# Kernel tuning notes

Measured on AMD Instinct MI355X. Metric: run time of the kernel, lower is better.

## Reference

```python
import jax, jax.numpy as jnp
import numpy as np

V = 8192
E = 262144
IN_DIM = 128
OUT_DIM = 128
NEG_SLOPE = 0.2


def setup_inputs() -> dict:
    key = jax.random.key(0)
    k1, k2, k3, k4 = jax.random.split(key, 4)
    h = jax.random.normal(k1, (V, IN_DIM), dtype=jnp.float32)
    edge_index = jax.random.randint(k2, (2, E), 0, V, dtype=jnp.int64)
    # nn.Linear weights: W (out_dim, in_dim), att (1, 2*out_dim), both bias-free
    W = jax.random.normal(k3, (OUT_DIM, IN_DIM), dtype=jnp.float32) / np.sqrt(IN_DIM)
    att_w = jax.random.normal(k4, (1, 2 * OUT_DIM), dtype=jnp.float32) / np.sqrt(2 * OUT_DIM)
    return {"h": h, "edge_index": edge_index, "W": W, "att_w": att_w}


def reference(h, edge_index, W, att_w):
    # h: (V, in_dim) -> (V, out_dim)
    hw = h @ W.T
    src, dst = edge_index[0], edge_index[1]
    # edge features: concat of endpoint embeddings -> (E, 2*out_dim)
    e = jnp.concatenate([hw[src], hw[dst]], axis=-1)
    # attention logits per edge, LeakyReLU(0.2)
    a = jax.nn.leaky_relu(jnp.squeeze(e @ att_w.T, -1), negative_slope=NEG_SLOPE)
    v = hw.shape[0]
    # faithful to original: dense V x V matrix, zeros on non-edges,
    # softmax over ALL columns (non-edges included as score 0)
    alpha = jnp.zeros((v, v), dtype=hw.dtype).at[src, dst].set(a)
    alpha = jax.nn.softmax(alpha, axis=-1)
    # dropout is identity in eval mode (deterministic reference)
    return alpha @ hw
```

## Files before the change

### kernel.cpp

```cpp
#include <hip/hip_runtime.h>
#include <hip/hip_bf16.h>
#include <math.h>


#define V 8192
#define E 262144
#define D 128
#define NEG_SLOPE 0.2f
#define CAP 96

#define FMA4(acc, hv, wv) { acc.x += (hv)*(wv).x; acc.y += (hv)*(wv).y; \
                            acc.z += (hv)*(wv).z; acc.w += (hv)*(wv).w; }

__global__ __launch_bounds__(256) void k_hw(const float* __restrict__ h,
                                            const float* __restrict__ W,
                                            const float* __restrict__ att,
                                            float* __restrict__ hw,
                                            float* __restrict__ s1,
                                            float* __restrict__ s2,
                                            float* __restrict__ S) {
    __shared__ float Wt[D * 132];
    __shared__ float hs[16][D];
    __shared__ float atts[2 * D];
    atts[threadIdx.x] = att[threadIdx.x];
    for (int e = threadIdx.x; e < D * D; e += 256) {
        int o = e >> 7, k = e & 127;
        Wt[k * 132 + o] = W[e];
    }
    int r0 = blockIdx.x * 16;
    for (int e = threadIdx.x; e < 16 * D; e += 256)
        hs[e >> 7][e & 127] = h[(r0 + (e >> 7)) * D + (e & 127)];
    __syncthreads();

    int c4 = (threadIdx.x & 31) * 4;
    int rq = threadIdx.x >> 5;
    float4 acc0 = make_float4(0.f, 0.f, 0.f, 0.f);
    float4 acc1 = make_float4(0.f, 0.f, 0.f, 0.f);
    #pragma unroll 2
    for (int kq = 0; kq < D; kq += 4) {
        float4 ha = *(const float4*)&hs[rq][kq];
        float4 hb = *(const float4*)&hs[rq + 8][kq];
        float4 w0 = *(const float4*)&Wt[(kq + 0) * 132 + c4];
        float4 w1 = *(const float4*)&Wt[(kq + 1) * 132 + c4];
        float4 w2 = *(const float4*)&Wt[(kq + 2) * 132 + c4];
        float4 w3 = *(const float4*)&Wt[(kq + 3) * 132 + c4];
        FMA4(acc0, ha.x, w0); FMA4(acc0, ha.y, w1);
        FMA4(acc0, ha.z, w2); FMA4(acc0, ha.w, w3);
        FMA4(acc1, hb.x, w0); FMA4(acc1, hb.y, w1);
        FMA4(acc1, hb.z, w2); FMA4(acc1, hb.w, w3);
    }
    int rowa = r0 + rq, rowb = r0 + rq + 8;
    *(float4*)&hw[rowa * D + c4] = acc0;
    *(float4*)&hw[rowb * D + c4] = acc1;

    float p1a = acc0.x * atts[c4] + acc0.y * atts[c4 + 1] + acc0.z * atts[c4 + 2] + acc0.w * atts[c4 + 3];
    float p2a = acc0.x * atts[D + c4] + acc0.y * atts[D + c4 + 1] + acc0.z * atts[D + c4 + 2] + acc0.w * atts[D + c4 + 3];
    float p1b = acc1.x * atts[c4] + acc1.y * atts[c4 + 1] + acc1.z * atts[c4 + 2] + acc1.w * atts[c4 + 3];
    float p2b = acc1.x * atts[D + c4] + acc1.y * atts[D + c4 + 1] + acc1.z * atts[D + c4 + 2] + acc1.w * atts[D + c4 + 3];
    #pragma unroll
    for (int m = 16; m; m >>= 1) {
        p1a += __shfl_xor(p1a, m); p2a += __shfl_xor(p2a, m);
        p1b += __shfl_xor(p1b, m); p2b += __shfl_xor(p2b, m);
    }
    if ((threadIdx.x & 31) == 0) {
        s1[rowa] = p1a; s2[rowa] = p2a;
        s1[rowb] = p1b; s2[rowb] = p2b;
    }

    __syncthreads();
    float* scr = &hs[0][0];
    scr[rq * D + c4 + 0] = acc0.x + acc1.x;
    scr[rq * D + c4 + 1] = acc0.y + acc1.y;
    scr[rq * D + c4 + 2] = acc0.z + acc1.z;
    scr[rq * D + c4 + 3] = acc0.w + acc1.w;
    __syncthreads();
    if (threadIdx.x < D) {
        float t = 0.f;
        #pragma unroll
        for (int r = 0; r < 8; ++r) t += scr[r * D + threadIdx.x];
        atomicAdd(&S[threadIdx.x], t);
    }
}

__global__ __launch_bounds__(256) void k_scatter(const int* __restrict__ ei,
                                                 const float* __restrict__ s1,
                                                 const float* __restrict__ s2,
                                                 int* __restrict__ cnt,
                                                 int2* __restrict__ bucket) {
    int t = blockIdx.x * 256 + threadIdx.x;
    int4 sv = *(const int4*)&ei[4 * t];
    int4 dv = *(const int4*)&ei[E + 4 * t];
    const int* sp = &sv.x;
    const int* dp = &dv.x;
    #pragma unroll
    for (int j = 0; j < 4; ++j) {
        int src = sp[j], dst = dp[j];
        float a = s1[src] + s2[dst];
        a = a > 0.f ? a : NEG_SLOPE * a;
        float w = expf(a) - 1.f;
        int pos = atomicAdd(&cnt[src], 1);
        if (pos < CAP)
            bucket[src * CAP + pos] = make_int2(dst, __float_as_int(w));
    }
}

__global__ __launch_bounds__(256) void k_row(const int2* __restrict__ bucket,
                                             const int* __restrict__ cnt,
                                             const float* __restrict__ hw,
                                             const float* __restrict__ S,
                                             float* __restrict__ out) {
    int row = (blockIdx.x * 256 + threadIdx.x) >> 6;
    int lane = threadIdx.x & 63;
    int deg = cnt[row];
    if (deg > CAP) deg = CAP;
    const int2* b = bucket + row * CAP;
    int2 e0 = b[lane];
    int2 e1 = (lane < CAP - 64) ? b[64 + lane] : make_int2(-1, 0);
    int   d0 = (lane < deg)      ? e0.x : -1;
    float w0 = (lane < deg)      ? __int_as_float(e0.y) : 0.f;
    int   d1 = (64 + lane < deg) ? e1.x : -1;
    float w1 = (64 + lane < deg) ? __int_as_float(e1.y) : 0.f;
    int n0 = deg < 64 ? deg : 64;

    bool dup0 = false, dup1 = false;
    for (int j = 0; j < n0; ++j) {
        int dj = __shfl(d0, j);
        dup0 |= (d0 == dj) & (lane > j);
        dup1 |= (d1 == dj);
    }
    for (int j = 64; j < deg; ++j) {
        int dj = __shfl(d1, j - 64);
        dup1 |= (d1 == dj) & (lane > j - 64);
    }
    if (dup0) w0 = 0.f;
    if (dup1) w1 = 0.f;

    float2 acc = make_float2(0.f, 0.f);
    float dex = 0.f;
    for (int j = 0; j < n0; ++j) {
        int   dj = __shfl(d0, j);
        float wj = __shfl(w0, j);
        float2 hv = *(const float2*)&hw[dj * D + lane * 2];
        acc.x += wj * hv.x; acc.y += wj * hv.y;
        dex += wj;
    }
    for (int j = 64; j < deg; ++j) {
        int   dj = __shfl(d1, j - 64);
        float wj = __shfl(w1, j - 64);
        float2 hv = *(const float2*)&hw[dj * D + lane * 2];
        acc.x += wj * hv.x; acc.y += wj * hv.y;
        dex += wj;
    }

    float inv = 1.f / ((float)V + dex);
    float2 s = *(const float2*)&S[lane * 2];
    float2 o;
    o.x = (s.x + acc.x) * inv;
    o.y = (s.y + acc.y) * inv;
    *(float2*)&out[row * D + lane * 2] = o;
}

extern "C" void kernel_launch(void* const* d_in, const int* in_sizes, int n_in,
                              void* d_out, int out_size, void* d_ws, size_t ws_size,
                              hipStream_t stream) {
    const float* h   = (const float*)d_in[0];
    const int*   ei  = (const int*)d_in[1];
    const float* W   = (const float*)d_in[2];
    const float* att = (const float*)d_in[3];
    float* out = (float*)d_out;

    char* ws = (char*)d_ws;
    float* hw  = (float*)(ws);
    float* s1  = (float*)(ws + 4194304);
    float* s2  = (float*)(ws + 4227072);
    float* S   = (float*)(ws + 4259840);
    int*   cnt = (int*)(ws + 4260352);
    int2*  bucket = (int2*)(ws + 4293120);

    hipMemsetAsync(ws + 4259840, 0, 512 + 32768, stream);

    k_hw     <<<512,  256, 0, stream>>>(h, W, att, hw, s1, s2, S);
    k_scatter<<<256,  256, 0, stream>>>(ei, s1, s2, cnt, bucket);
    k_row    <<<2048, 256, 0, stream>>>(bucket, cnt, hw, S, out);
}
```

Measured before the change: 119.3 us.

## Fuse GAT pipeline into one cooperative kernel with grid syncs

Replaces the memset plus three kernel launches with a single cooperative kernel of 1024 blocks that runs init, hw projection, edge scatter and row aggregation as phases separated by grid-wide syncs. Launch overhead and the memset go away. The projection now reads h directly from global memory and splits K across waves, reducing through shared memory. The column-sum reduction now writes per-block partials that are folded during the scatter phase, replacing the per-block atomics. The gains depend on grid.sync being cheaper than kernel boundaries and on all 1024 blocks being co-resident; if the cooperative launch fails, it falls back to four separate launches.

```diff
diff --git a/kernel.cpp b/kernel.cpp
--- a/kernel.cpp
+++ b/kernel.cpp
@@ -1,6 +1,9 @@
 #include <hip/hip_runtime.h>
+#include <hip/hip_cooperative_groups.h>
 #include <hip/hip_bf16.h>
 #include <math.h>
+
+namespace cg = cooperative_groups;
 
 
 #define V 8192
@@ -8,156 +11,208 @@
 #define D 128
 #define NEG_SLOPE 0.2f
 #define CAP 96
-
-#define FMA4(acc, hv, wv) { acc.x += (hv)*(wv).x; acc.y += (hv)*(wv).y; \
-                            acc.z += (hv)*(wv).z; acc.w += (hv)*(wv).w; }
-
-__global__ __launch_bounds__(256) void k_hw(const float* __restrict__ h,
-                                            const float* __restrict__ W,
-                                            const float* __restrict__ att,
-                                            float* __restrict__ hw,
-                                            float* __restrict__ s1,
-                                            float* __restrict__ s2,
-                                            float* __restrict__ S) {
-    __shared__ float Wt[D * 132];
-    __shared__ float hs[16][D];
-    __shared__ float atts[2 * D];
-    atts[threadIdx.x] = att[threadIdx.x];
-    for (int e = threadIdx.x; e < D * D; e += 256) {
-        int o = e >> 7, k = e & 127;
-        Wt[k * 132 + o] = W[e];
-    }
-    int r0 = blockIdx.x * 16;
-    for (int e = threadIdx.x; e < 16 * D; e += 256)
-        hs[e >> 7][e & 127] = h[(r0 + (e >> 7)) * D + (e & 127)];
+#define NB 1024
+
+__device__ __forceinline__ void phase_init(const float* __restrict__ W,
+                                           float* __restrict__ Wt,
+                                           int* __restrict__ cnt,
+                                           float* __restrict__ S) {
+    int g = blockIdx.x * 256 + threadIdx.x;
+    if (g < D * D) {
+        int o = g >> 7, k = g & 127;
+        Wt[k * D + o] = W[g];
+    } else if (g < D * D + V) {
+        cnt[g - D * D] = 0;
+    } else if (g < D * D + V + D) {
+        S[g - D * D - V] = 0.f;
+    }
+}
+
+__device__ __forceinline__ void phase_hw(const float* __restrict__ h,
+                                         const float* __restrict__ Wt,
+                                         const float* __restrict__ att,
+                                         float* __restrict__ hw,
+                                         float* __restrict__ s1,
+                                         float* __restrict__ s2,
+                                         float* __restrict__ Pb,
+                                         float* scr) {
+    int r0 = blockIdx.x * 8;
+    int wv = threadIdx.x >> 6;
+    int lane = threadIdx.x & 63;
+    int c2 = lane * 2;
+    int ks = wv * 32;
+    float2 acc[8];
+    #pragma unroll
+    for (int r = 0; r < 8; ++r) acc[r] = make_float2(0.f, 0.f);
+    #pragma unroll 2
+    for (int kc = 0; kc < 32; kc += 4) {
+        int k = ks + kc;
+        float2 w0 = *(const float2*)&Wt[(k + 0) * D + c2];
+        float2 w1 = *(const float2*)&Wt[(k + 1) * D + c2];
+        float2 w2 = *(const float2*)&Wt[(k + 2) * D + c2];
+        float2 w3 = *(const float2*)&Wt[(k + 3) * D + c2];
+        #pragma unroll
+        for (int r = 0; r < 8; ++r) {
+            float4 hv = *(const float4*)&h[(r0 + r) * D + k];
+            acc[r].x += hv.x * w0.x + hv.y * w1.x + hv.z * w2.x + hv.w * w3.x;
+            acc[r].y += hv.x * w0.y + hv.y * w1.y + hv.z * w2.y + hv.w * w3.y;
+        }
+    }
+    #pragma unroll
+    for (int r = 0; r < 8; ++r)
+        *(float2*)&scr[(wv * 8 + r) * D + c2] = acc[r];
     __syncthreads();
-
+    int rq = threadIdx.x >> 5;
     int c4 = (threadIdx.x & 31) * 4;
-    int rq = threadIdx.x >> 5;
-    float4 acc0 = make_float4(0.f, 0.f, 0.f, 0.f);
-    float4 acc1 = make_float4(0.f, 0.f, 0.f, 0.f);
-    #pragma unroll 2
-    for (int kq = 0; kq < D; kq += 4) {
-        float4 ha = *(const float4*)&hs[rq][kq];
-        float4 hb = *(const float4*)&hs[rq + 8][kq];
-        float4 w0 = *(const float4*)&Wt[(kq + 0) * 132 + c4];
-        float4 w1 = *(const float4*)&Wt[(kq + 1) * 132 + c4];
-        float4 w2 = *(const float4*)&Wt[(kq + 2) * 132 + c4];
-        float4 w3 = *(const float4*)&Wt[(kq + 3) * 132 + c4];
-        FMA4(acc0, ha.x, w0); FMA4(acc0, ha.y, w1);
-        FMA4(acc0, ha.z, w2); FMA4(acc0, ha.w, w3);
-        FMA4(acc1, hb.x, w0); FMA4(acc1, hb.y, w1);
-        FMA4(acc1, hb.z, w2); FMA4(acc1, hb.w, w3);
-    }
-    int rowa = r0 + rq, rowb = r0 + rq + 8;
-    *(float4*)&hw[rowa * D + c4] = acc0;
-    *(float4*)&hw[rowb * D + c4] = acc1;
-
-    float p1a = acc0.x * atts[c4] + acc0.y * atts[c4 + 1] + acc0.z * atts[c4 + 2] + acc0.w * atts[c4 + 3];
-    float p2a = acc0.x * atts[D + c4] + acc0.y * atts[D + c4 + 1] + acc0.z * atts[D + c4 + 2] + acc0.w * atts[D + c4 + 3];
-    float p1b = acc1.x * atts[c4] + acc1.y * atts[c4 + 1] + acc1.z * atts[c4 + 2] + acc1.w * atts[c4 + 3];
-    float p2b = acc1.x * atts[D + c4] + acc1.y * atts[D + c4 + 1] + acc1.z * atts[D + c4 + 2] + acc1.w * atts[D + c4 + 3];
-    #pragma unroll
-    for (int m = 16; m; m >>= 1) {
-        p1a += __shfl_xor(p1a, m); p2a += __shfl_xor(p2a, m);
-        p1b += __shfl_xor(p1b, m); p2b += __shfl_xor(p2b, m);
-    }
-    if ((threadIdx.x & 31) == 0) {
-        s1[rowa] = p1a; s2[rowa] = p2a;
-        s1[rowb] = p1b; s2[rowb] = p2b;
-    }
-
+    float4 v = make_float4(0.f, 0.f, 0.f, 0.f);
+    #pragma unroll
+    for (int w = 0; w < 4; ++w) {
+        float4 p = *(const float4*)&scr[(w * 8 + rq) * D + c4];
+        v.x += p.x; v.y += p.y; v.z += p.z; v.w += p.w;
+    }
+    int row = r0 + rq;
+    *(float4*)&hw[row * D + c4] = v;
+    float4 a1 = *(const float4*)&att[c4];
+    float4 a2 = *(const float4*)&att[D + c4];
+    float p1 = v.x * a1.x + v.y * a1.y + v.z * a1.z + v.w * a1.w;
+    float p2 = v.x * a2.x + v.y * a2.y + v.z * a2.z + v.w * a2.w;
+    #pragma unroll
+    for (int m = 16; m; m >>= 1) { p1 += __shfl_xor(p1, m); p2 += __shfl_xor(p2, m); }
+    if ((threadIdx.x & 31) == 0) { s1[row] = p1; s2[row] = p2; }
     __syncthreads();
-    float* scr = &hs[0][0];
-    scr[rq * D + c4 + 0] = acc0.x + acc1.x;
-    scr[rq * D + c4 + 1] = acc0.y + acc1.y;
-    scr[rq * D + c4 + 2] = acc0.z + acc1.z;
-    scr[rq * D + c4 + 3] = acc0.w + acc1.w;
+    *(float4*)&scr[rq * D + c4] = v;
     __syncthreads();
-    if (threadIdx.x < D) {
+    if (rq == 0) {
+        float4 t = make_float4(0.f, 0.f, 0.f, 0.f);
+        #pragma unroll
+        for (int r = 0; r < 8; ++r) {
+            float4 p = *(const float4*)&scr[r * D + c4];
+            t.x += p.x; t.y += p.y; t.z += p.z; t.w += p.w;
+        }
+        *(float4*)&Pb[blockIdx.x * D + c4] = t;
+    }
+}
+
+__device__ __forceinline__ void phase_scatter(const int* __restrict__ ei,
+                                              const float* __restrict__ s1,
+                                              const float* __restrict__ s2,
+                                              int* __restrict__ cnt,
+                                              int2* __restrict__ bucket,
+                                              const float* __restrict__ Pb,
+                                              float* __restrict__ S,
+                                              float* scr) {
+    int e = blockIdx.x * 256 + threadIdx.x;
+    int src = ei[e];
+    int dst = ei[E + e];
+    float a = s1[src] + s2[dst];
+    a = a > 0.f ? a : NEG_SLOPE * a;
+    float w = expf(a) - 1.f;
+    int pos = atomicAdd(&cnt[src], 1);
+    if (pos < CAP)
+        bucket[src * CAP + pos] = make_int2(dst, __float_as_int(w));
+    if (blockIdx.x < 8) {
+        int c = threadIdx.x & 127;
+        int rh = threadIdx.x >> 7;
         float t = 0.f;
-        #pragma unroll
-        for (int r = 0; r < 8; ++r) t += scr[r * D + threadIdx.x];
-        atomicAdd(&S[threadIdx.x], t);
-    }
-}
-
-__global__ __launch_bounds__(256) void k_scatter(const int* __restrict__ ei,
-                                                 const float* __restrict__ s1,
-                                                 const float* __restrict__ s2,
-                                                 int* __restrict__ cnt,
-                                                 int2* __restrict__ bucket) {
-    int t = blockIdx.x * 256 + threadIdx.x;
-    int4 sv = *(const int4*)&ei[4 * t];
-    int4 dv = *(const int4*)&ei[E + 4 * t];
-    const int* sp = &sv.x;
-    const int* dp = &dv.x;
-    #pragma unroll
-    for (int j = 0; j < 4; ++j) {
-        int src = sp[j], dst = dp[j];
-        float a = s1[src] + s2[dst];
-        a = a > 0.f ? a : NEG_SLOPE * a;
-        float w = expf(a) - 1.f;
-        int pos = atomicAdd(&cnt[src], 1);
-        if (pos < CAP)
-            bucket[src * CAP + pos] = make_int2(dst, __float_as_int(w));
-    }
-}
-
-__global__ __launch_bounds__(256) void k_row(const int2* __restrict__ bucket,
-                                             const int* __restrict__ cnt,
-                                             const float* __restrict__ hw,
-                                             const float* __restrict__ S,
-                                             float* __restrict__ out) {
-    int row = (blockIdx.x * 256 + threadIdx.x) >> 6;
+        int rbase = blockIdx.x * (NB / 8);
+        for (int r = rh; r < NB / 8; r += 2)
+            t += Pb[(rbase + r) * D + c];
+        scr[threadIdx.x] = t;
+        __syncthreads();
+        if (threadIdx.x < D)
+            atomicAdd(&S[c], scr[c] + scr[D + c]);
+    }
+}
+
+__device__ __forceinline__ void phase_row(const int2* __restrict__ bucket,
+                                          const int* __restrict__ cnt,
+                                          const float* __restrict__ hw,
+                                          const float* __restrict__ S,
+                                          float* __restrict__ out) {
+    int gw = (blockIdx.x * 256 + threadIdx.x) >> 6;
     int lane = threadIdx.x & 63;
-    int deg = cnt[row];
-    if (deg > CAP) deg = CAP;
-    const int2* b = bucket + row * CAP;
-    int2 e0 = b[lane];
-    int2 e1 = (lane < CAP - 64) ? b[64 + lane] : make_int2(-1, 0);
-    int   d0 = (lane < deg)      ? e0.x : -1;
-    float w0 = (lane < deg)      ? __int_as_float(e0.y) : 0.f;
-    int   d1 = (64 + lane < deg) ? e1.x : -1;
-    float w1 = (64 + lane < deg) ? __int_as_float(e1.y) : 0.f;
-    int n0 = deg < 64 ? deg : 64;
-
-    bool dup0 = false, dup1 = false;
-    for (int j = 0; j < n0; ++j) {
-        int dj = __shfl(d0, j);
-        dup0 |= (d0 == dj) & (lane > j);
-        dup1 |= (d1 == dj);
-    }
-    for (int j = 64; j < deg; ++j) {
-        int dj = __shfl(d1, j - 64);
-        dup1 |= (d1 == dj) & (lane > j - 64);
-    }
-    if (dup0) w0 = 0.f;
-    if (dup1) w1 = 0.f;
-
-    float2 acc = make_float2(0.f, 0.f);
-    float dex = 0.f;
-    for (int j = 0; j < n0; ++j) {
-        int   dj = __shfl(d0, j);
-        float wj = __shfl(w0, j);
-        float2 hv = *(const float2*)&hw[dj * D + lane * 2];
-        acc.x += wj * hv.x; acc.y += wj * hv.y;
-        dex += wj;
-    }
-    for (int j = 64; j < deg; ++j) {
-        int   dj = __shfl(d1, j - 64);
-        float wj = __shfl(w1, j - 64);
-        float2 hv = *(const float2*)&hw[dj * D + lane * 2];
-        acc.x += wj * hv.x; acc.y += wj * hv.y;
-        dex += wj;
-    }
-
-    float inv = 1.f / ((float)V + dex);
     float2 s = *(const float2*)&S[lane * 2];
-    float2 o;
-    o.x = (s.x + acc.x) * inv;
-    o.y = (s.y + acc.y) * inv;
-    *(float2*)&out[row * D + lane * 2] = o;
+    for (int rr = 0; rr < 2; ++rr) {
+        int row = gw * 2 + rr;
+        int deg = cnt[row];
+        if (deg > CAP) deg = CAP;
+        const int2* b = bucket + row * CAP;
+        int2 e0 = b[lane];
+        int2 e1 = (lane < CAP - 64) ? b[64 + lane] : make_int2(-1, 0);
+        int   d0 = (lane < deg)      ? e0.x : -1;
+        float w0 = (lane < deg)      ? __int_as_float(e0.y) : 0.f;
+        int   d1 = (64 + lane < deg) ? e1.x : -1;
+        float w1 = (64 + lane < deg) ? __int_as_float(e1.y) : 0.f;
+        int n0 = deg < 64 ? deg : 64;
+        bool dup0 = false, dup1 = false;
+        for (int j = 0; j < n0; ++j) {
+            int dj = __shfl(d0, j);
+            dup0 |= (d0 == dj) & (lane > j);
+            dup1 |= (d1 == dj);
+        }
+        for (int j = 64; j < deg; ++j) {
+            int dj = __shfl(d1, j - 64);
+            dup1 |= (d1 == dj) & (lane > j - 64);
+        }
+        if (dup0) w0 = 0.f;
+        if (dup1) w1 = 0.f;
+        float2 acc = make_float2(0.f, 0.f);
+        float dex = 0.f;
+        for (int j = 0; j < n0; ++j) {
+            int   dj = __shfl(d0, j);
+            float wj = __shfl(w0, j);
+            float2 hv = *(const float2*)&hw[dj * D + lane * 2];
+            acc.x += wj * hv.x; acc.y += wj * hv.y;
+            dex += wj;
+        }
+        for (int j = 64; j < deg; ++j) {
+            int   dj = __shfl(d1, j - 64);
+            float wj = __shfl(w1, j - 64);
+            float2 hv = *(const float2*)&hw[dj * D + lane * 2];
+            acc.x += wj * hv.x; acc.y += wj * hv.y;
+            dex += wj;
+        }
+        float inv = 1.f / ((float)V + dex);
+        float2 o;
+        o.x = (s.x + acc.x) * inv;
+        o.y = (s.y + acc.y) * inv;
+        *(float2*)&out[row * D + lane * 2] = o;
+    }
+}
+
+__global__ __launch_bounds__(256, 4) void k_gat_coop(
+        const float* __restrict__ h, const int* __restrict__ ei,
+        const float* __restrict__ W, const float* __restrict__ att,
+        float* __restrict__ hw, float* __restrict__ s1, float* __restrict__ s2,
+        float* __restrict__ S, int* __restrict__ cnt, int2* __restrict__ bucket,
+        float* __restrict__ Wt, float* __restrict__ Pb, float* __restrict__ out) {
+    __shared__ float scr[4 * 8 * D];
+    cg::grid_group g = cg::this_grid();
+    phase_init(W, Wt, cnt, S);
+    g.sync();
+    phase_hw(h, Wt, att, hw, s1, s2, Pb, scr);
+    g.sync();
+    phase_scatter(ei, s1, s2, cnt, bucket, Pb, S, scr);
+    g.sync();
+    phase_row(bucket, cnt, hw, S, out);
+}
+
+__global__ __launch_bounds__(256, 4) void k_init_f(const float* W, float* Wt, int* cnt, float* S) {
+    phase_init(W, Wt, cnt, S);
+}
+__global__ __launch_bounds__(256, 4) void k_hw_f(const float* h, const float* Wt, const float* att,
+        float* hw, float* s1, float* s2, float* Pb) {
+    __shared__ float scr[4 * 8 * D];
+    phase_hw(h, Wt, att, hw, s1, s2, Pb, scr);
+}
+__global__ __launch_bounds__(256, 4) void k_sc_f(const int* ei, const float* s1, const float* s2,
+        int* cnt, int2* bucket, const float* Pb, float* S) {
+    __shared__ float scr[4 * 8 * D];
+    phase_scatter(ei, s1, s2, cnt, bucket, Pb, S, scr);
+}
+__global__ __launch_bounds__(256, 4) void k_row_f(const int2* bucket, const int* cnt,
+        const float* hw, const float* S, float* out) {
+    phase_row(bucket, cnt, hw, S, out);
 }
 
 extern "C" void kernel_launch(void* const* d_in, const int* in_sizes, int n_in,
@@ -176,10 +231,18 @@
     float* S   = (float*)(ws + 4259840);
     int*   cnt = (int*)(ws + 4260352);
     int2*  bucket = (int2*)(ws + 4293120);
-
-    hipMemsetAsync(ws + 4259840, 0, 512 + 32768, stream);
-
-    k_hw     <<<512,  256, 0, stream>>>(h, W, att, hw, s1, s2, S);
-    k_scatter<<<256,  256, 0, stream>>>(ei, s1, s2, cnt, bucket);
-    k_row    <<<2048, 256, 0, stream>>>(bucket, cnt, hw, S, out);
-}
+    float* Wt  = (float*)(ws + 10584576);
+    float* Pb  = (float*)(ws + 10650112);
+
+    void* args[] = {(void*)&h, (void*)&ei, (void*)&W, (void*)&att, (void*)&hw,
+                    (void*)&s1, (void*)&s2, (void*)&S, (void*)&cnt, (void*)&bucket,
+                    (void*)&Wt, (void*)&Pb, (void*)&out};
+    hipError_t err = hipLaunchCooperativeKernel((const void*)k_gat_coop,
+                                                dim3(NB), dim3(256), args, 0, stream);
+    if (err != hipSuccess) {
+        k_init_f<<<NB, 256, 0, stream>>>(W, Wt, cnt, S);
+        k_hw_f  <<<NB, 256, 0, stream>>>(h, Wt, att, hw, s1, s2, Pb);
+        k_sc_f  <<<NB, 256, 0, stream>>>(ei, s1, s2, cnt, bucket, Pb, S);
+        k_row_f <<<NB, 256, 0, stream>>>(bucket, cnt, hw, S, out);
+    }
+}
```

Result: slower. 440.6 us (+269.4%).

## Store hw and edge weights in bf16, drop memset, fuse dedup into gather

Applied to the files above, without the earlier changes.

Projected features are stored as bf16 and each bucket entry packs dst and a bf16 weight into one int, which halves the gather and bucket traffic. The memset goes away: counts are zeroed inside k_hw, and the column-sum atomics become per-block partials reduced by an extra block in the scatter kernel. Duplicate-edge detection moves from a separate shuffle loop into a ballot inside the accumulation loop. The cost is bf16 precision on hw and on the weights, and packing dst into 16 bits only works because V is at most 65536.

```diff
diff --git a/kernel.cpp b/kernel.cpp
--- a/kernel.cpp
+++ b/kernel.cpp
@@ -12,28 +12,47 @@
 #define FMA4(acc, hv, wv) { acc.x += (hv)*(wv).x; acc.y += (hv)*(wv).y; \
                             acc.z += (hv)*(wv).z; acc.w += (hv)*(wv).w; }
 
+__device__ __forceinline__ unsigned short f2bf(float f) {
+    unsigned u = __float_as_uint(f);
+    return (unsigned short)((u + 0x7fffu + ((u >> 16) & 1u)) >> 16);
+}
+__device__ __forceinline__ float bf2f_low(int p) {
+    return __uint_as_float(((unsigned)p) << 16);
+}
+
 __global__ __launch_bounds__(256) void k_hw(const float* __restrict__ h,
                                             const float* __restrict__ W,
                                             const float* __restrict__ att,
-                                            float* __restrict__ hw,
+                                            unsigned short* __restrict__ hwb,
                                             float* __restrict__ s1,
                                             float* __restrict__ s2,
-                                            float* __restrict__ S) {
+                                            float* __restrict__ Pb,
+                                            int* __restrict__ cnt) {
     __shared__ float Wt[D * 132];
     __shared__ float hs[16][D];
     __shared__ float atts[2 * D];
-    atts[threadIdx.x] = att[threadIdx.x];
-    for (int e = threadIdx.x; e < D * D; e += 256) {
-        int o = e >> 7, k = e & 127;
-        Wt[k * 132 + o] = W[e];
-    }
-    int r0 = blockIdx.x * 16;
-    for (int e = threadIdx.x; e < 16 * D; e += 256)
-        hs[e >> 7][e & 127] = h[(r0 + (e >> 7)) * D + (e & 127)];
+    int t = threadIdx.x, b = blockIdx.x;
+    int g0 = b * 256 + t;
+    if (g0 < V) cnt[g0] = 0;
+    atts[t] = att[t];
+    for (int f4 = t; f4 < (D * D) / 4; f4 += 256) {
+        int o = f4 >> 5, k = (f4 * 4) & 127;
+        float4 wv = *(const float4*)&W[o * D + k];
+        Wt[(k + 0) * 132 + o] = wv.x;
+        Wt[(k + 1) * 132 + o] = wv.y;
+        Wt[(k + 2) * 132 + o] = wv.z;
+        Wt[(k + 3) * 132 + o] = wv.w;
+    }
+    int r0 = b * 16;
+    {
+        int row = t >> 5, col = (t * 4) & 127;
+        *(float4*)&hs[row][col]     = *(const float4*)&h[(r0 + row) * D + col];
+        *(float4*)&hs[row + 8][col] = *(const float4*)&h[(r0 + row + 8) * D + col];
+    }
     __syncthreads();
 
-    int c4 = (threadIdx.x & 31) * 4;
-    int rq = threadIdx.x >> 5;
+    int c4 = (t & 31) * 4;
+    int rq = t >> 5;
     float4 acc0 = make_float4(0.f, 0.f, 0.f, 0.f);
     float4 acc1 = make_float4(0.f, 0.f, 0.f, 0.f);
     #pragma unroll 2
@@ -50,8 +69,10 @@
         FMA4(acc1, hb.z, w2); FMA4(acc1, hb.w, w3);
     }
     int rowa = r0 + rq, rowb = r0 + rq + 8;
-    *(float4*)&hw[rowa * D + c4] = acc0;
-    *(float4*)&hw[rowb * D + c4] = acc1;
+    ushort4 pa = make_ushort4(f2bf(acc0.x), f2bf(acc0.y), f2bf(acc0.z), f2bf(acc0.w));
+    ushort4 pb = make_ushort4(f2bf(acc1.x), f2bf(acc1.y), f2bf(acc1.z), f2bf(acc1.w));
+    *(ushort4*)&hwb[rowa * D + c4] = pa;
+    *(ushort4*)&hwb[rowb * D + c4] = pb;
 
     float p1a = acc0.x * atts[c4] + acc0.y * atts[c4 + 1] + acc0.z * atts[c4 + 2] + acc0.w * atts[c4 + 3];
     float p2a = acc0.x * atts[D + c4] + acc0.y * atts[D + c4 + 1] + acc0.z * atts[D + c4 + 2] + acc0.w * atts[D + c4 + 3];
@@ -62,7 +83,7 @@
         p1a += __shfl_xor(p1a, m); p2a += __shfl_xor(p2a, m);
         p1b += __shfl_xor(p1b, m); p2b += __shfl_xor(p2b, m);
     }
-    if ((threadIdx.x & 31) == 0) {
+    if ((t & 31) == 0) {
         s1[rowa] = p1a; s2[rowa] = p2a;
         s1[rowb] = p1b; s2[rowb] = p2b;
     }
@@ -74,11 +95,11 @@
     scr[rq * D + c4 + 2] = acc0.z + acc1.z;
     scr[rq * D + c4 + 3] = acc0.w + acc1.w;
     __syncthreads();
-    if (threadIdx.x < D) {
-        float t = 0.f;
+    if (t < D) {
+        float s = 0.f;
         #pragma unroll
-        for (int r = 0; r < 8; ++r) t += scr[r * D + threadIdx.x];
-        atomicAdd(&S[threadIdx.x], t);
+        for (int r = 0; r < 8; ++r) s += scr[r * D + t];
+        Pb[b * D + t] = s;
     }
 }
 
@@ -86,72 +107,82 @@
                                                  const float* __restrict__ s1,
                                                  const float* __restrict__ s2,
                                                  int* __restrict__ cnt,
-                                                 int2* __restrict__ bucket) {
-    int t = blockIdx.x * 256 + threadIdx.x;
-    int4 sv = *(const int4*)&ei[4 * t];
-    int4 dv = *(const int4*)&ei[E + 4 * t];
-    const int* sp = &sv.x;
-    const int* dp = &dv.x;
-    #pragma unroll
-    for (int j = 0; j < 4; ++j) {
-        int src = sp[j], dst = dp[j];
-        float a = s1[src] + s2[dst];
-        a = a > 0.f ? a : NEG_SLOPE * a;
-        float w = expf(a) - 1.f;
-        int pos = atomicAdd(&cnt[src], 1);
-        if (pos < CAP)
-            bucket[src * CAP + pos] = make_int2(dst, __float_as_int(w));
-    }
-}
-
-__global__ __launch_bounds__(256) void k_row(const int2* __restrict__ bucket,
+                                                 int* __restrict__ bucket,
+                                                 const float* __restrict__ Pb,
+                                                 float* __restrict__ S) {
+    int b = blockIdx.x, t = threadIdx.x;
+    if (b < 256) {
+        int g = b * 256 + t;
+        int4 sv = *(const int4*)&ei[4 * g];
+        int4 dv = *(const int4*)&ei[E + 4 * g];
+        const int* sp = &sv.x;
+        const int* dp = &dv.x;
+        #pragma unroll
+        for (int j = 0; j < 4; ++j) {
+            int src = sp[j], dst = dp[j];
+            float a = s1[src] + s2[dst];
+            a = a > 0.f ? a : NEG_SLOPE * a;
+            float w = expf(a) - 1.f;
+            int pos = atomicAdd(&cnt[src], 1);
+            if (pos < CAP)
+                bucket[src * CAP + pos] = (dst << 16) | (int)f2bf(w);
+        }
+    } else {
+        __shared__ float red[256];
+        int c = t & 127, half = t >> 7;
+        float s = 0.f;
+        #pragma unroll 4
+        for (int r = half; r < 512; r += 2)
+            s += Pb[r * D + c];
+        red[t] = s;
+        __syncthreads();
+        if (t < D) S[t] = red[t] + red[D + t];
+    }
+}
+
+__global__ __launch_bounds__(256) void k_row(const int* __restrict__ bucket,
                                              const int* __restrict__ cnt,
-                                             const float* __restrict__ hw,
+                                             const unsigned short* __restrict__ hwb,
                                              const float* __restrict__ S,
                                              float* __restrict__ out) {
-    int row = (blockIdx.x * 256 + threadIdx.x) >> 6;
-    int lane = threadIdx.x & 63;
+    int t = threadIdx.x;
+    int wv = t >> 6, lane = t & 63;
+    int row = blockIdx.x * 4 + wv;
     int deg = cnt[row];
     if (deg > CAP) deg = CAP;
-    const int2* b = bucket + row * CAP;
-    int2 e0 = b[lane];
-    int2 e1 = (lane < CAP - 64) ? b[64 + lane] : make_int2(-1, 0);
-    int   d0 = (lane < deg)      ? e0.x : -1;
-    float w0 = (lane < deg)      ? __int_as_float(e0.y) : 0.f;
-    int   d1 = (64 + lane < deg) ? e1.x : -1;
-    float w1 = (64 + lane < deg) ? __int_as_float(e1.y) : 0.f;
+    const int* bk = bucket + row * CAP;
+    int e0 = bk[lane];
+    int e1 = (lane < CAP - 64) ? bk[64 + lane] : 0;
+    int p0 = (lane < deg)      ? e0 : (int)0xFFFF0000;
+    int p1 = (64 + lane < deg) ? e1 : (int)0xFFFF0000;
+    int d0 = p0 >> 16;
+    int d1 = p1 >> 16;
     int n0 = deg < 64 ? deg : 64;
-
-    bool dup0 = false, dup1 = false;
-    for (int j = 0; j < n0; ++j) {
-        int dj = __shfl(d0, j);
-        dup0 |= (d0 == dj) & (lane > j);
-        dup1 |= (d1 == dj);
-    }
-    for (int j = 64; j < deg; ++j) {
-        int dj = __shfl(d1, j - 64);
-        dup1 |= (d1 == dj) & (lane > j - 64);
-    }
-    if (dup0) w0 = 0.f;
-    if (dup1) w1 = 0.f;
-
     float2 acc = make_float2(0.f, 0.f);
     float dex = 0.f;
     for (int j = 0; j < n0; ++j) {
-        int   dj = __shfl(d0, j);
-        float wj = __shfl(w0, j);
-        float2 hv = *(const float2*)&hw[dj * D + lane * 2];
-        acc.x += wj * hv.x; acc.y += wj * hv.y;
+        int pj = __shfl(p0, j);
+        int dj = pj >> 16;
+        float wj = bf2f_low(pj);
+        unsigned long long m = __ballot(d0 == dj);
+        if (m & ((1ull << j) - 1ull)) wj = 0.f;
+        unsigned hv = *(const unsigned*)&hwb[dj * D + lane * 2];
+        acc.x += wj * __uint_as_float(hv << 16);
+        acc.y += wj * __uint_as_float(hv & 0xFFFF0000u);
         dex += wj;
     }
     for (int j = 64; j < deg; ++j) {
-        int   dj = __shfl(d1, j - 64);
-        float wj = __shfl(w1, j - 64);
-        float2 hv = *(const float2*)&hw[dj * D + lane * 2];
-        acc.x += wj * hv.x; acc.y += wj * hv.y;
+        int pj = __shfl(p1, j - 64);
+        int dj = pj >> 16;
+        float wj = bf2f_low(pj);
+        unsigned long long m0 = __ballot(d0 == dj);
+        unsigned long long m1 = __ballot(d1 == dj) & ((1ull << (j - 64)) - 1ull);
+        if (m0 | m1) wj = 0.f;
+        unsigned hv = *(const unsigned*)&hwb[dj * D + lane * 2];
+        acc.x += wj * __uint_as_float(hv << 16);
+        acc.y += wj * __uint_as_float(hv & 0xFFFF0000u);
         dex += wj;
     }
-
     float inv = 1.f / ((float)V + dex);
     float2 s = *(const float2*)&S[lane * 2];
     float2 o;
@@ -170,16 +201,15 @@
     float* out = (float*)d_out;
 
     char* ws = (char*)d_ws;
-    float* hw  = (float*)(ws);
-    float* s1  = (float*)(ws + 4194304);
-    float* s2  = (float*)(ws + 4227072);
-    float* S   = (float*)(ws + 4259840);
-    int*   cnt = (int*)(ws + 4260352);
-    int2*  bucket = (int2*)(ws + 4293120);
-
-    hipMemsetAsync(ws + 4259840, 0, 512 + 32768, stream);
-
-    k_hw     <<<512,  256, 0, stream>>>(h, W, att, hw, s1, s2, S);
-    k_scatter<<<256,  256, 0, stream>>>(ei, s1, s2, cnt, bucket);
-    k_row    <<<2048, 256, 0, stream>>>(bucket, cnt, hw, S, out);
-}
+    unsigned short* hwb = (unsigned short*)(ws);
+    float* s1  = (float*)(ws + 2097152);
+    float* s2  = (float*)(ws + 2129920);
+    float* S   = (float*)(ws + 2162688);
+    int*   cnt = (int*)(ws + 2163200);
+    int*   bucket = (int*)(ws + 2195968);
+    float* Pb  = (float*)(ws + 5341696);
+
+    k_hw     <<<512,  256, 0, stream>>>(h, W, att, hwb, s1, s2, Pb, cnt);
+    k_scatter<<<257,  256, 0, stream>>>(ei, s1, s2, cnt, bucket, Pb, S);
+    k_row    <<<2048, 256, 0, stream>>>(bucket, cnt, hwb, S, out);
+}
```

New measurement: 118.2 us. Within noise of the previous version (-0.9%).
